# Optimization experiments

Hardware: AMD Instinct MI355X
Metric: run time of the kernel (lower is better)

Reference implementation:

```python
import jax, jax.numpy as jnp
import numpy as np

NEG_SLOPE = 0.2  # PyG GATConv leaky_relu slope


def _gat_conv(x, src, dst, W, a_s, a_d, b, H, D, concat):
    """PyG-style GATConv (eval mode, self-loops already in src/dst).
    x: [N, F_in], W: [F_in, H*D], a_s/a_d: [H, D], b: [H*D] or [D]."""
    N = x.shape[0]
    h = (x @ W).reshape(N, H, D)                      # [N, H, D]
    al_src = (h * a_s).sum(-1)                        # [N, H]
    al_dst = (h * a_d).sum(-1)                        # [N, H]
    e = jax.nn.leaky_relu(al_src[src] + al_dst[dst], NEG_SLOPE)   # [E, H]
    m = jax.ops.segment_max(e, dst, num_segments=N)               # [N, H]
    m = jnp.where(jnp.isfinite(m), m, 0.0)
    ex = jnp.exp(e - m[dst])
    denom = jax.ops.segment_sum(ex, dst, num_segments=N)
    alpha = ex / (denom[dst] + 1e-16)                 # edge softmax per dst node
    out = jax.ops.segment_sum(alpha[:, :, None] * h[src], dst, num_segments=N)  # [N, H, D]
    out = out.reshape(N, H * D) if concat else out.mean(axis=1)
    return out + b


def setup_inputs() -> dict:
    key = jax.random.key(0)
    ks = jax.random.split(key, 14)
    N, E, F_in, H, D, OUT = 50000, 800000, 256, 8, 32, 64
    g = lambda k, shape, fan: (jax.random.normal(k, shape, jnp.float32) / np.float32(np.sqrt(fan)))
    return {
        "x": jax.random.normal(ks[0], (N, F_in), jnp.float32),
        "edge_index": jax.random.randint(ks[1], (2, E), 0, N),
        # conv0: GATConv(256 -> 32, heads=8, concat)
        "W0": g(ks[2], (F_in, H * D), F_in),
        "a_src0": g(ks[3], (H, D), D),
        "a_dst0": g(ks[4], (H, D), D),
        "b0": jnp.zeros((H * D,), jnp.float32),
        # residual0: Linear(256 -> 256)
        "Wr0": g(ks[5], (F_in, H * D), F_in),
        "br0": jnp.zeros((H * D,), jnp.float32),
        # conv1: GATConv(256 -> 64, heads=1, concat=False)
        "W1": g(ks[6], (H * D, OUT), H * D),
        "a_src1": g(ks[7], (1, OUT), OUT),
        "a_dst1": g(ks[8], (1, OUT), OUT),
        "b1": jnp.zeros((OUT,), jnp.float32),
        # residual1: Linear(256 -> 64)
        "Wr1": g(ks[9], (H * D, OUT), H * D),
        "br1": jnp.zeros((OUT,), jnp.float32),
    }


def reference(x, edge_index, W0, a_src0, a_dst0, b0, Wr0, br0, W1, a_src1, a_dst1, b1, Wr1, br1):
    N = x.shape[0]
    loops = jnp.arange(N, dtype=edge_index.dtype)
    src = jnp.concatenate([edge_index[0], loops])   # add self loops
    dst = jnp.concatenate([edge_index[1], loops])
    # layer 0: GATConv + residual + ELU (dropout is identity in eval)
    h = _gat_conv(x, src, dst, W0, a_src0, a_dst0, b0, 8, 32, True)
    h = jax.nn.elu(h + (x @ Wr0 + br0))
    # final layer: heads=1, concat=False, + residual
    out = _gat_conv(h, src, dst, W1, a_src1, a_dst1, b1, 1, 64, False)
    out = out + (h @ Wr1 + br1)
    return jax.nn.log_softmax(out, axis=1)
```

## Files before the change

kernel.cpp:

```cpp
#include <hip/hip_runtime.h>
#include <math.h>

#define NEG_SLOPE 0.2f
#define BSH 7
#define NBLK_PART 256

typedef __attribute__((ext_vector_type(8))) short bf16x8;
typedef __attribute__((ext_vector_type(4))) float f32x4;
typedef __attribute__((ext_vector_type(2))) float f32x2;
typedef __attribute__((ext_vector_type(8))) unsigned short ushort8;
typedef __attribute__((ext_vector_type(4))) unsigned short ushort4v;

__device__ __forceinline__ float b2f(unsigned short u){
  return __uint_as_float(((unsigned)u) << 16);
}
__device__ __forceinline__ unsigned short f2b(float f){
  unsigned u = __float_as_uint(f);
  return (unsigned short)((u + 0x7FFFu + ((u >> 16) & 1u)) >> 16);
}

#if __has_builtin(__builtin_amdgcn_cvt_pk_f32_fp8) && __has_builtin(__builtin_amdgcn_cvt_pk_fp8_f32)
#define HW_FP8 1
#else
#define HW_FP8 0
#endif

#if !HW_FP8
__device__ __forceinline__ unsigned enc8_one(float f){
  unsigned bits = __float_as_uint(f);
  unsigned s = bits >> 31;
  unsigned e = (bits >> 23) & 255;
  unsigned mant = bits & 0x7FFFFF;
  if(e < 121){
    float af = fabsf(f);
    int m = (int)(af * 512.f + 0.5f);
    if(m > 7) m = 7;
    return (s << 7) | (unsigned)m;
  }
  unsigned lsb = (mant >> 20) & 1;
  mant += 0x7FFFF + lsb;
  if(mant >> 23){ e += 1; mant = 0; }
  unsigned m3 = mant >> 20;
  unsigned e8 = e - 120;
  if(e8 > 15 || (e8 == 15 && m3 == 7)) return (s << 7) | 0x7E;
  return (s << 7) | (e8 << 3) | m3;
}
#endif

template<bool HI>
__device__ __forceinline__ unsigned enc8_pair(float a, float b, unsigned old){
#if HW_FP8
  return __builtin_amdgcn_cvt_pk_fp8_f32(a, b, old, HI);
#else
  unsigned p = enc8_one(a) | (enc8_one(b) << 8);
  return HI ? ((old & 0x0000FFFFu) | (p << 16)) : ((old & 0xFFFF0000u) | p);
#endif
}

__device__ __forceinline__ void dec8x4v(unsigned q, f32x2& lo, f32x2& hi){
#if HW_FP8
  lo = __builtin_amdgcn_cvt_pk_f32_fp8(q, false);
  hi = __builtin_amdgcn_cvt_pk_f32_fp8(q, true);
#else
  auto dec1 = [](unsigned b)->float{
    unsigned s = (b >> 7) & 1, e = (b >> 3) & 15, m = b & 7;
    float v = (e == 0) ? (float)m * 0.001953125f
                       : __uint_as_float(((e + 120) << 23) | (m << 20));
    return s ? -v : v;
  };
  lo[0] = dec1(q & 255); lo[1] = dec1((q >> 8) & 255);
  hi[0] = dec1((q >> 16) & 255); hi[1] = dec1(q >> 24);
#endif
}

extern "C" __global__ void k_part1(const int* __restrict__ dsts, int E, int N,
                                   int NBUCK, int* __restrict__ bcnt,
                                   int* __restrict__ blockbase){
  __shared__ int hist[512];
  int blk = blockIdx.x, tid = threadIdx.x;
  for(int b = tid; b < NBUCK; b += 256) hist[b] = 0;
  __syncthreads();
  int ET = E + N;
  int chunk = (ET + NBLK_PART - 1)/NBLK_PART;
  int s0 = blk*chunk, s1 = s0+chunk < ET ? s0+chunk : ET;
  for(int e = s0+tid; e < s1; e += 256){
    int d = (e < E) ? dsts[e] : e - E;
    atomicAdd(&hist[d >> BSH], 1);
  }
  __syncthreads();
  for(int b = tid; b < NBUCK; b += 256)
    blockbase[(size_t)blk*NBUCK + b] = atomicAdd(&bcnt[b], hist[b]);
}

extern "C" __global__ void k_bscan(const int* __restrict__ bcnt, int* __restrict__ boffs,
                                   int* __restrict__ offs_last, int NBUCK, int ET){
  __shared__ int sc[512], orig[512];
  int t = threadIdx.x;
  int v = (t < NBUCK) ? bcnt[t] : 0;
  sc[t] = v; orig[t] = v;
  __syncthreads();
  for(int st=1; st<512; st<<=1){
    int u = (t >= st) ? sc[t-st] : 0;
    __syncthreads();
    sc[t] += u;
    __syncthreads();
  }
  if(t < NBUCK) boffs[t] = sc[t] - orig[t];
  if(t == 0){ boffs[NBUCK] = ET; *offs_last = ET; }
}

extern "C" __global__ void k_part2(const int* __restrict__ srcs, const int* __restrict__ dsts,
                                   int E, int N, int NBUCK,
                                   const int* __restrict__ boffs, const int* __restrict__ blockbase,
                                   uint2* __restrict__ pairs){
  __shared__ int cur[512];
  int blk = blockIdx.x, tid = threadIdx.x;
  for(int b = tid; b < NBUCK; b += 256)
    cur[b] = boffs[b] + blockbase[(size_t)blk*NBUCK + b];
  __syncthreads();
  int ET = E + N;
  int chunk = (ET + NBLK_PART - 1)/NBLK_PART;
  int s0 = blk*chunk, s1 = s0+chunk < ET ? s0+chunk : ET;
  for(int e = s0+tid; e < s1; e += 256){
    int s, d;
    if(e < E){ s = srcs[e]; d = dsts[e]; } else { s = d = e - E; }
    int pos = atomicAdd(&cur[d >> BSH], 1);
    uint2 pr; pr.x = (unsigned)d; pr.y = (unsigned)s;
    pairs[pos] = pr;
  }
}

extern "C" __global__ void k_bcsr(const uint2* __restrict__ pairs, const int* __restrict__ boffs,
                                  int N, int* __restrict__ offs, int* __restrict__ csr){
  __shared__ int hist[128], sc[128], lcur[128];
  int b = blockIdx.x, tid = threadIdx.x;
  int node0 = b << BSH;
  int base = boffs[b], endp = boffs[b+1];
  if(tid < 128) hist[tid] = 0;
  __syncthreads();
  for(int i = base + tid; i < endp; i += 256)
    atomicAdd(&hist[pairs[i].x & 127], 1);
  __syncthreads();
  if(tid < 128) sc[tid] = hist[tid];
  __syncthreads();
  for(int st=1; st<128; st<<=1){
    int u = (tid < 128 && tid >= st) ? sc[tid-st] : 0;
    __syncthreads();
    if(tid < 128) sc[tid] += u;
    __syncthreads();
  }
  if(tid < 128){
    int ex = sc[tid] - hist[tid];
    lcur[tid] = ex;
    int n = node0 + tid;
    if(n < N) offs[n] = base + ex;
  }
  __syncthreads();
  for(int i = base + tid; i < endp; i += 256){
    uint2 pr = pairs[i];
    int pos = atomicAdd(&lcur[pr.x & 127], 1);
    csr[base + pos] = (int)pr.y;
  }
}

extern "C" __global__ void k_wt2(const float* __restrict__ W0, const float* __restrict__ Wr0,
                                 const float* __restrict__ W1, const float* __restrict__ Wr1,
                                 unsigned short* __restrict__ WT0, unsigned short* __restrict__ WT1){
  int idx = blockIdx.x*256 + threadIdx.x;
  const int tot0 = 512*256;
  if(idx < tot0){
    int n = idx >> 8, k = idx & 255;
    const float* W = (n < 256) ? W0 : Wr0;
    int c = (n < 256) ? n : n - 256;
    WT0[idx] = f2b(W[(size_t)k*256 + c]);
  } else {
    idx -= tot0;
    if(idx >= 128*256) return;
    int n = idx >> 8, k = idx & 255;
    const float* W = (n < 64) ? W1 : Wr1;
    int c = (n < 64) ? n : n - 64;
    WT1[idx] = f2b(W[(size_t)k*64 + c]);
  }
}

__launch_bounds__(256)
extern "C" __global__ void k_mgemm(const unsigned short* __restrict__ A,
                                   const float* __restrict__ Afp,
                                   const unsigned short* __restrict__ WT,
                                   unsigned short* __restrict__ C, int M,
                                   int MB, int NCB, int mode,
                                   unsigned char* __restrict__ qout,
                                   unsigned short* __restrict__ rout,
                                   const float* __restrict__ as0v, const float* __restrict__ ad0v,
                                   float* __restrict__ alsout, float* __restrict__ aldout){
  int id = blockIdx.x;
  int row_blk, col_blk;
  if(NCB == 4){
    int group = id >> 5;
    int r8 = id & 7;
    col_blk = (id >> 3) & 3;
    row_blk = group*8 + r8;
  } else {
    row_blk = id; col_blk = 0;
  }
  if(row_blk >= MB) return;

  __shared__ unsigned short SH[128*128];
  unsigned short* As = SH;
  unsigned short* Bs = SH + 128*64;
  int t = threadIdx.x;
  int lane = t & 63, wid = t >> 6;
  int wr = wid >> 1, wc = wid & 1;
  int row0 = row_blk*128, col0 = col_blk*128;
  f32x4 acc[4][4] = {};

  float4 v0s[4], v1s[4];
  const float* abase[4];
  if(Afp){
    #pragma unroll
    for(int i=0; i<4; i++){
      int t2 = i*256 + t;
      int r = t2 >> 3;
      int dslot = (t2 & 7) ^ (r & 7);
      int gr = row0 + r; if(gr >= M) gr = M - 1;
      abase[i] = Afp + (size_t)gr*256 + dslot*8;
      v0s[i] = *(const float4*)(abase[i]);
      v1s[i] = *(const float4*)(abase[i] + 4);
    }
  }

  for(int k0 = 0; k0 < 256; k0 += 64){
    if(Afp){
      #pragma unroll
      for(int i=0; i<4; i++){
        ushort8 o;
        o[0]=f2b(v0s[i].x); o[1]=f2b(v0s[i].y); o[2]=f2b(v0s[i].z); o[3]=f2b(v0s[i].w);
        o[4]=f2b(v1s[i].x); o[5]=f2b(v1s[i].y); o[6]=f2b(v1s[i].z); o[7]=f2b(v1s[i].w);
        *(ushort8*)(As + i*2048 + wid*512 + lane*8) = o;
      }
    } else {
      #pragma unroll
      for(int i=0; i<4; i++){
        int t2 = i*256 + t;
        int r = t2 >> 3;
        int dslot = (t2 & 7) ^ (r & 7);
        int gr = row0 + r; if(gr >= M) gr = M - 1;
        const unsigned short* ga = A + (size_t)gr*256 + k0 + dslot*8;
        __builtin_amdgcn_global_load_lds((const __attribute__((address_space(1))) unsigned*)ga,
            (__attribute__((address_space(3))) unsigned*)(As + i*2048 + wid*512), 16, 0, 0);
      }
    }
    #pragma unroll
    for(int i=0; i<4; i++){
      int t2 = i*256 + t;
      int r = t2 >> 3;
      int dslot = (t2 & 7) ^ (r & 7);
      const unsigned short* gb = WT + (size_t)(col0 + r)*256 + k0 + dslot*8;
      __builtin_amdgcn_global_load_lds((const __attribute__((address_space(1))) unsigned*)gb,
          (__attribute__((address_space(3))) unsigned*)(Bs + i*2048 + wid*512), 16, 0, 0);
    }
    __syncthreads();
    if(Afp && k0 < 192){
      #pragma unroll
      for(int i=0; i<4; i++){
        v0s[i] = *(const float4*)(abase[i] + k0 + 64);
        v1s[i] = *(const float4*)(abase[i] + k0 + 68);
      }
    }
    #pragma unroll
    for(int kc=0; kc<2; kc++){
      bf16x8 a[4], b[4];
      int kb = kc*4 + (lane >> 4);
      #pragma unroll
      for(int f=0; f<4; f++){
        int ar = wr*64 + f*16 + (lane & 15);
        a[f] = *(const bf16x8*)&As[ar*64 + ((kb ^ (ar & 7))*8)];
        int br = wc*64 + f*16 + (lane & 15);
        b[f] = *(const bf16x8*)&Bs[br*64 + ((kb ^ (br & 7))*8)];
      }
      #pragma unroll
      for(int fm=0; fm<4; fm++)
        #pragma unroll
        for(int fn=0; fn<4; fn++)
          acc[fm][fn] = __builtin_amdgcn_mfma_f32_16x16x32_bf16(a[fm], b[fn], acc[fm][fn], 0, 0, 0);
    }
    __syncthreads();
  }

  #pragma unroll
  for(int fm=0; fm<4; fm++){
    int rl = wr*64 + fm*16 + ((lane>>4)<<2);
    #pragma unroll
    for(int r=0; r<4; r++)
      #pragma unroll
      for(int fn=0; fn<4; fn++)
        SH[(rl+r)*128 + wc*64 + (lane&15) + fn*16] = f2b(acc[fm][fn][r]);
  }
  __syncthreads();

  int cg = t & 15;
  if(mode == 0){
    bool attn = col_blk < 2;
    int colbase = col0 + cg*8;
    float4 as_lo, as_hi, ad_lo, ad_hi;
    if(attn){
      as_lo = *(const float4*)(as0v + colbase);
      as_hi = *(const float4*)(as0v + colbase + 4);
      ad_lo = *(const float4*)(ad0v + colbase);
      ad_hi = *(const float4*)(ad0v + colbase + 4);
    }
    #pragma unroll
    for(int it=0; it<8; it++){
      int rl = it*16 + (t>>4);
      int row = row0 + rl;
      ushort8 vr = *(ushort8*)&SH[rl*128 + cg*8];
      if(attn){
        float f0=b2f(vr[0]),f1=b2f(vr[1]),f2=b2f(vr[2]),f3=b2f(vr[3]);
        float f4=b2f(vr[4]),f5=b2f(vr[5]),f6=b2f(vr[6]),f7=b2f(vr[7]);
        float sd = f0*as_lo.x+f1*as_lo.y+f2*as_lo.z+f3*as_lo.w
                 + f4*as_hi.x+f5*as_hi.y+f6*as_hi.z+f7*as_hi.w;
        float dd = f0*ad_lo.x+f1*ad_lo.y+f2*ad_lo.z+f3*ad_lo.w
                 + f4*ad_hi.x+f5*ad_hi.y+f6*ad_hi.z+f7*ad_hi.w;
        sd += __shfl_xor(sd,1); sd += __shfl_xor(sd,2);
        dd += __shfl_xor(dd,1); dd += __shfl_xor(dd,2);
        uint2 q;
        q.x = enc8_pair<false>(f0,f1,0u); q.x = enc8_pair<true>(f2,f3,q.x);
        q.y = enc8_pair<false>(f4,f5,0u); q.y = enc8_pair<true>(f6,f7,q.y);
        if(row < M){
          *(uint2*)(qout + (size_t)row*256 + colbase) = q;
          if((lane&3)==0){
            int head = colbase >> 5;
            alsout[row*8 + head] = sd;
            aldout[row*8 + head] = dd;
          }
        }
      } else {
        if(row < M)
          *(ushort8*)(rout + (size_t)row*256 + (colbase - 256)) = vr;
      }
    }
  } else {
    #pragma unroll
    for(int it=0; it<8; it++){
      int rl = it*16 + (t>>4);
      int row = row0 + rl;
      ushort8 vr = *(ushort8*)&SH[rl*128 + cg*8];
      if(row < M){
        *(ushort8*)(C + (size_t)row*128 + cg*8) = vr;
        if(cg < 8){
          float f0=b2f(vr[0]),f1=b2f(vr[1]),f2=b2f(vr[2]),f3=b2f(vr[3]);
          float f4=b2f(vr[4]),f5=b2f(vr[5]),f6=b2f(vr[6]),f7=b2f(vr[7]);
          uint2 q;
          q.x = enc8_pair<false>(f0,f1,0u); q.x = enc8_pair<true>(f2,f3,q.x);
          q.y = enc8_pair<false>(f4,f5,0u); q.y = enc8_pair<true>(f6,f7,q.y);
          *(uint2*)(qout + (size_t)row*64 + cg*8) = q;
        }
      }
    }
  }
}

__launch_bounds__(256)
extern "C" __global__ void k_gather0(const unsigned short* __restrict__ r0b,
                                     const unsigned char* __restrict__ h0q,
                                     const float* __restrict__ als0, const float* __restrict__ ald0,
                                     const int* __restrict__ offs, const int* __restrict__ csr,
                                     const float* __restrict__ b0, const float* __restrict__ br0,
                                     unsigned short* __restrict__ h1b, int N){
  int n = blockIdx.x*4 + (threadIdx.x >> 6);
  if(n >= N) return;
  int lane = threadIdx.x & 63;
  int hh = lane & 7;
  int es = lane >> 3;
  int h  = es;
  int c  = lane*4;
  float ald_h = ald0[n*8 + hh];
  int beg = offs[n], end = offs[n+1];

  f32x2 A01 = {0.f, 0.f}, A23 = {0.f, 0.f};
  float den = 0.f;

  for(int chunk = beg; chunk < end; chunk += 8){
    int m = end - chunk; if(m > 8) m = 8;
    bool e_ok = es < m;
    int s = e_ok ? csr[chunk + es] : 0;
    float p = 0.f;
    if(e_ok){
      float v = als0[s*8 + hh] + ald_h;
      v = v > 0.f ? v : NEG_SLOPE*v;
      p = expf(v);
    }
    den += p;
    int sj[8]; float pj[8];
    #pragma unroll
    for(int j=0; j<8; j++){
      sj[j] = __shfl(s, j*8);
      pj[j] = __shfl(p, j*8 + h);
    }
    unsigned q[8];
    #pragma unroll
    for(int j=0; j<8; j++)
      q[j] = *(const unsigned*)(h0q + (size_t)sj[j]*256 + c);
    #pragma unroll
    for(int j=0; j<8; j++){
      f32x2 lo, hi, pv;
      dec8x4v(q[j], lo, hi);
      pv[0] = pj[j]; pv[1] = pj[j];
      A01 += pv*lo; A23 += pv*hi;
    }
  }

  den += __shfl_xor(den, 8);
  den += __shfl_xor(den, 16);
  den += __shfl_xor(den, 32);
  float rden = 1.f/(den + 1e-16f);
  rden = __shfl(rden, h);

  float a0 = A01[0]*rden, a1 = A01[1]*rden, a2 = A23[0]*rden, a3 = A23[1]*rden;

  float4 bb = *(const float4*)(b0 + c);
  float4 rb = *(const float4*)(br0 + c);
  uint2 ru = *(const uint2*)(r0b + (size_t)n*256 + c);
  float o0 = a0 + bb.x + __uint_as_float(ru.x << 16)         + rb.x;
  float o1 = a1 + bb.y + __uint_as_float(ru.x & 0xFFFF0000u) + rb.y;
  float o2 = a2 + bb.z + __uint_as_float(ru.y << 16)         + rb.z;
  float o3 = a3 + bb.w + __uint_as_float(ru.y & 0xFFFF0000u) + rb.w;
  ushort4v o;
  o[0] = f2b(o0 > 0.f ? o0 : expf(o0) - 1.f);
  o[1] = f2b(o1 > 0.f ? o1 : expf(o1) - 1.f);
  o[2] = f2b(o2 > 0.f ? o2 : expf(o2) - 1.f);
  o[3] = f2b(o3 > 0.f ? o3 : expf(o3) - 1.f);
  *(ushort4v*)(h1b + (size_t)n*256 + c) = o;
}

extern "C" __global__ void k_al1(const unsigned short* __restrict__ buf1b, const float* __restrict__ as1,
                                 const float* __restrict__ ad1, float* als1, float* ald1, int N){
  int n = blockIdx.x*4 + (threadIdx.x >> 6);
  if(n >= N) return;
  int lane = threadIdx.x & 63;
  float g = b2f(buf1b[(size_t)n*128 + lane]);
  float s = g*as1[lane], d = g*ad1[lane];
  #pragma unroll
  for(int o=32; o>0; o>>=1){ s += __shfl_xor(s,o); d += __shfl_xor(d,o); }
  if(lane == 0){ als1[n] = s; ald1[n] = d; }
}

__launch_bounds__(256)
extern "C" __global__ void k_gather1(const unsigned short* __restrict__ buf1b,
                                     const unsigned char* __restrict__ g1q,
                                     const float* __restrict__ als1, const float* __restrict__ ald1,
                                     const int* __restrict__ offs, const int* __restrict__ csr,
                                     const float* __restrict__ b1, const float* __restrict__ br1,
                                     float* __restrict__ out, int N){
  int n = blockIdx.x*4 + (threadIdx.x >> 6);
  if(n >= N) return;
  int lane = threadIdx.x & 63;
  int ch4 = lane & 15;
  int es  = lane >> 4;
  int c   = ch4*4;
  int beg = offs[n], end = offs[n+1];
  float ald_n = ald1[n];

  f32x2 A01 = {0.f, 0.f}, A23 = {0.f, 0.f};
  float den = 0.f;

  for(int chunk = beg; chunk < end; chunk += 64){
    int m = end - chunk; if(m > 64) m = 64;
    int s = (lane < m) ? csr[chunk + lane] : 0;
    float p = 0.f;
    if(lane < m){
      float v = als1[s] + ald_n;
      v = v > 0.f ? v : NEG_SLOPE*v;
      p = expf(v);
    }
    den += p;
    for(int base = 0; base < m; base += 16){
      int sv[4]; float pv[4];
      #pragma unroll
      for(int i=0; i<4; i++){
        int j = base + 4*i + es;
        int jj = j & 63;
        sv[i] = __shfl(s, jj);
        pv[i] = __shfl(p, jj);
      }
      unsigned qv[4];
      #pragma unroll
      for(int i=0; i<4; i++)
        qv[i] = *(const unsigned*)(g1q + (size_t)sv[i]*64 + c);
      #pragma unroll
      for(int i=0; i<4; i++){
        f32x2 lo, hi, pp;
        dec8x4v(qv[i], lo, hi);
        pp[0] = pv[i]; pp[1] = pv[i];
        A01 += pp*lo; A23 += pp*hi;
      }
    }
  }

  A01[0] += __shfl_xor(A01[0], 16); A01[1] += __shfl_xor(A01[1], 16);
  A23[0] += __shfl_xor(A23[0], 16); A23[1] += __shfl_xor(A23[1], 16);
  A01[0] += __shfl_xor(A01[0], 32); A01[1] += __shfl_xor(A01[1], 32);
  A23[0] += __shfl_xor(A23[0], 32); A23[1] += __shfl_xor(A23[1], 32);
  #pragma unroll
  for(int o=32; o>0; o>>=1) den += __shfl_xor(den, o);
  float rden = 1.f/(den + 1e-16f);

  float4 bb = *(const float4*)(b1 + c);
  float4 rb = *(const float4*)(br1 + c);
  uint2 ru = *(const uint2*)(buf1b + (size_t)n*128 + 64 + c);
  float v0 = A01[0]*rden + bb.x + __uint_as_float(ru.x << 16)         + rb.x;
  float v1 = A01[1]*rden + bb.y + __uint_as_float(ru.x & 0xFFFF0000u) + rb.y;
  float v2 = A23[0]*rden + bb.z + __uint_as_float(ru.y << 16)         + rb.z;
  float v3 = A23[1]*rden + bb.w + __uint_as_float(ru.y & 0xFFFF0000u) + rb.w;

  float mx = fmaxf(fmaxf(v0, v1), fmaxf(v2, v3));
  #pragma unroll
  for(int o=1; o<16; o<<=1) mx = fmaxf(mx, __shfl_xor(mx, o));
  float sm = expf(v0-mx) + expf(v1-mx) + expf(v2-mx) + expf(v3-mx);
  #pragma unroll
  for(int o=1; o<16; o<<=1) sm += __shfl_xor(sm, o);
  float l = mx + logf(sm);
  if(es == 0){
    float4 ov; ov.x = v0-l; ov.y = v1-l; ov.z = v2-l; ov.w = v3-l;
    *(float4*)(out + (size_t)n*64 + c) = ov;
  }
}

extern "C" void kernel_launch(void* const* d_in, const int* in_sizes, int n_in,
                              void* d_out, int out_size, void* d_ws, size_t ws_size,
                              hipStream_t stream){
  const float* x   = (const float*)d_in[0];
  const int*   ei  = (const int*)  d_in[1];
  const float* W0  = (const float*)d_in[2];
  const float* as0 = (const float*)d_in[3];
  const float* ad0 = (const float*)d_in[4];
  const float* b0  = (const float*)d_in[5];
  const float* Wr0 = (const float*)d_in[6];
  const float* br0 = (const float*)d_in[7];
  const float* W1  = (const float*)d_in[8];
  const float* as1 = (const float*)d_in[9];
  const float* ad1 = (const float*)d_in[10];
  const float* b1  = (const float*)d_in[11];
  const float* Wr1 = (const float*)d_in[12];
  const float* br1 = (const float*)d_in[13];
  int N = in_sizes[0] / 256;
  int E = in_sizes[1] / 2;
  const int* srcs = ei;
  const int* dsts = ei + E;
  float* out = (float*)d_out;

  int ET = E + N;
  int NBUCK = (N + 127) >> BSH;

  unsigned short* r0b   = (unsigned short*)d_ws;
  unsigned char*  h0q   = (unsigned char*)(r0b + (size_t)N*256);
  unsigned short* h1b   = (unsigned short*)(h0q + (size_t)N*256);
  unsigned short* buf1b = h1b + (size_t)N*256;
  unsigned short* WT0   = buf1b + (size_t)N*128;
  unsigned short* WT1   = WT0   + 512*256;
  float*    als0 = (float*)(WT1 + 128*256);
  float*    ald0 = als0 + (size_t)N*8;
  float*    als1 = ald0 + (size_t)N*8;
  float*    ald1 = als1 + N;
  int*      offs = (int*)(ald1 + N);
  int*      bcnt = offs + N + 1;
  int*      boffs = bcnt + NBUCK;
  int*      blockbase = boffs + NBUCK + 1;
  int*      csr  = blockbase + (size_t)NBLK_PART*NBUCK;
  uint2*    pairs = (uint2*)(csr + ET);
  pairs = (uint2*)(((uintptr_t)pairs + 7) & ~(uintptr_t)7);
  unsigned char* g1q = (unsigned char*)(pairs + ET);

  hipMemsetAsync(bcnt, 0, (size_t)NBUCK*sizeof(int), stream);
  hipLaunchKernelGGL(k_part1, dim3(NBLK_PART), dim3(256), 0, stream, dsts, E, N, NBUCK, bcnt, blockbase);
  hipLaunchKernelGGL(k_bscan, dim3(1), dim3(512), 0, stream, bcnt, boffs, offs + N, NBUCK, ET);
  hipLaunchKernelGGL(k_part2, dim3(NBLK_PART), dim3(256), 0, stream, srcs, dsts, E, N, NBUCK, boffs, blockbase, pairs);
  hipLaunchKernelGGL(k_bcsr, dim3(NBUCK), dim3(256), 0, stream, pairs, boffs, N, offs, csr);

  hipLaunchKernelGGL(k_wt2, dim3((512*256+128*256+255)/256), dim3(256), 0, stream, W0, Wr0, W1, Wr1, WT0, WT1);

  int MB = (N + 127) / 128;
  int g0 = ((MB + 7) / 8) * 32;
  hipLaunchKernelGGL(k_mgemm, dim3(g0), dim3(256), 0, stream,
                     (const unsigned short*)nullptr, x, WT0,
                     (unsigned short*)nullptr, N, MB, 4, 0,
                     h0q, r0b, as0, ad0, als0, ald0);
  hipLaunchKernelGGL(k_gather0, dim3((N+3)/4), dim3(256), 0, stream, r0b, h0q, als0, ald0, offs, csr, b0, br0, h1b, N);

  hipLaunchKernelGGL(k_mgemm, dim3(MB), dim3(256), 0, stream,
                     h1b, (const float*)nullptr, WT1,
                     buf1b, N, MB, 1, 1,
                     g1q, (unsigned short*)nullptr,
                     (const float*)nullptr, (const float*)nullptr,
                     (float*)nullptr, (float*)nullptr);
  hipLaunchKernelGGL(k_al1, dim3((N+3)/4), dim3(256), 0, stream, buf1b, as1, ad1, als1, ald1, N);
  hipLaunchKernelGGL(k_gather1, dim3((N+3)/4), dim3(256), 0, stream, buf1b, g1q, als1, ald1, offs, csr, b1, br1, out, N);
}
```

Measured before the change: 181.4 us.

## Load GEMM B fragments straight to registers, shrink LDS, fuse layer-1 attention logits

The GEMM now keeps the weight (B) operand in registers, loading MFMA fragments directly from global memory with a one-step prefetch, and stages only A through a smaller LDS buffer. The epilogue is split into two halves so the output tile fits in the reduced LDS. The layer-1 attention-logit computation (k_al1) is folded into the second GEMM's epilogue, which removes one kernel launch and a re-read of buf1b. Together these aim to raise occupancy and cut LDS traffic, at the cost of more scattered global loads for B and extra barriers in the epilogue.

```diff
diff --git a/kernel.cpp b/kernel.cpp
--- a/kernel.cpp
+++ b/kernel.cpp
@@ -184,49 +184,58 @@
 }
 
 __launch_bounds__(256)
-extern "C" __global__ void k_mgemm(const unsigned short* __restrict__ A,
+extern "C" __global__ void k_mgemm(const unsigned short* __restrict__ Ab,
                                    const float* __restrict__ Afp,
                                    const unsigned short* __restrict__ WT,
                                    unsigned short* __restrict__ C, int M,
                                    int MB, int NCB, int mode,
                                    unsigned char* __restrict__ qout,
                                    unsigned short* __restrict__ rout,
-                                   const float* __restrict__ as0v, const float* __restrict__ ad0v,
+                                   const float* __restrict__ asv, const float* __restrict__ adv,
                                    float* __restrict__ alsout, float* __restrict__ aldout){
   int id = blockIdx.x;
   int row_blk, col_blk;
   if(NCB == 4){
-    int group = id >> 5;
-    int r8 = id & 7;
     col_blk = (id >> 3) & 3;
-    row_blk = group*8 + r8;
+    row_blk = (id >> 5)*8 + (id & 7);
   } else {
     row_blk = id; col_blk = 0;
   }
   if(row_blk >= MB) return;
 
-  __shared__ unsigned short SH[128*128];
+  __shared__ unsigned short SH[64*136];
   unsigned short* As = SH;
-  unsigned short* Bs = SH + 128*64;
   int t = threadIdx.x;
   int lane = t & 63, wid = t >> 6;
   int wr = wid >> 1, wc = wid & 1;
   int row0 = row_blk*128, col0 = col_blk*128;
   f32x4 acc[4][4] = {};
 
-  float4 v0s[4], v1s[4];
-  const float* abase[4];
-  if(Afp){
-    #pragma unroll
-    for(int i=0; i<4; i++){
-      int t2 = i*256 + t;
-      int r = t2 >> 3;
-      int dslot = (t2 & 7) ^ (r & 7);
-      int gr = row0 + r; if(gr >= M) gr = M - 1;
-      abase[i] = Afp + (size_t)gr*256 + dslot*8;
-      v0s[i] = *(const float4*)(abase[i]);
-      v1s[i] = *(const float4*)(abase[i] + 4);
-    }
+  float4 va0[4], va1[4];
+  bf16x8 au[4];
+  const float* afp_ptr[4];
+  const unsigned short* ab_ptr[4];
+  #pragma unroll
+  for(int i=0; i<4; i++){
+    int t2 = i*256 + t;
+    int r = t2 >> 3, dslot = (t2 & 7) ^ (r & 7);
+    int gr = row0 + r; if(gr >= M) gr = M - 1;
+    if(Afp){
+      afp_ptr[i] = Afp + (size_t)gr*256 + dslot*8;
+      va0[i] = *(const float4*)afp_ptr[i];
+      va1[i] = *(const float4*)(afp_ptr[i] + 4);
+    } else {
+      ab_ptr[i] = Ab + (size_t)gr*256 + dslot*8;
+      au[i] = *(const bf16x8*)ab_ptr[i];
+    }
+  }
+  bf16x8 bcur[4], bnxt[4];
+  const unsigned short* bptr[4];
+  #pragma unroll
+  for(int f=0; f<4; f++){
+    int br = wc*64 + f*16 + (lane & 15);
+    bptr[f] = WT + (size_t)(col0 + br)*256 + (lane >> 4)*8;
+    bcur[f] = *(const bf16x8*)bptr[f];
   }
 
   for(int k0 = 0; k0 < 256; k0 += 64){
@@ -234,126 +243,147 @@
       #pragma unroll
       for(int i=0; i<4; i++){
         ushort8 o;
-        o[0]=f2b(v0s[i].x); o[1]=f2b(v0s[i].y); o[2]=f2b(v0s[i].z); o[3]=f2b(v0s[i].w);
-        o[4]=f2b(v1s[i].x); o[5]=f2b(v1s[i].y); o[6]=f2b(v1s[i].z); o[7]=f2b(v1s[i].w);
-        *(ushort8*)(As + i*2048 + wid*512 + lane*8) = o;
+        o[0]=f2b(va0[i].x); o[1]=f2b(va0[i].y); o[2]=f2b(va0[i].z); o[3]=f2b(va0[i].w);
+        o[4]=f2b(va1[i].x); o[5]=f2b(va1[i].y); o[6]=f2b(va1[i].z); o[7]=f2b(va1[i].w);
+        *(ushort8*)(As + i*2048 + t*8) = o;
       }
     } else {
       #pragma unroll
-      for(int i=0; i<4; i++){
-        int t2 = i*256 + t;
-        int r = t2 >> 3;
-        int dslot = (t2 & 7) ^ (r & 7);
-        int gr = row0 + r; if(gr >= M) gr = M - 1;
-        const unsigned short* ga = A + (size_t)gr*256 + k0 + dslot*8;
-        __builtin_amdgcn_global_load_lds((const __attribute__((address_space(1))) unsigned*)ga,
-            (__attribute__((address_space(3))) unsigned*)(As + i*2048 + wid*512), 16, 0, 0);
+      for(int i=0; i<4; i++)
+        *(bf16x8*)(As + i*2048 + t*8) = au[i];
+    }
+    __syncthreads();
+    if(k0 < 192){
+      if(Afp){
+        #pragma unroll
+        for(int i=0; i<4; i++){
+          va0[i] = *(const float4*)(afp_ptr[i] + k0 + 64);
+          va1[i] = *(const float4*)(afp_ptr[i] + k0 + 68);
+        }
+      } else {
+        #pragma unroll
+        for(int i=0; i<4; i++)
+          au[i] = *(const bf16x8*)(ab_ptr[i] + k0 + 64);
       }
     }
     #pragma unroll
-    for(int i=0; i<4; i++){
-      int t2 = i*256 + t;
-      int r = t2 >> 3;
-      int dslot = (t2 & 7) ^ (r & 7);
-      const unsigned short* gb = WT + (size_t)(col0 + r)*256 + k0 + dslot*8;
-      __builtin_amdgcn_global_load_lds((const __attribute__((address_space(1))) unsigned*)gb,
-          (__attribute__((address_space(3))) unsigned*)(Bs + i*2048 + wid*512), 16, 0, 0);
-    }
-    __syncthreads();
-    if(Afp && k0 < 192){
-      #pragma unroll
-      for(int i=0; i<4; i++){
-        v0s[i] = *(const float4*)(abase[i] + k0 + 64);
-        v1s[i] = *(const float4*)(abase[i] + k0 + 68);
-      }
-    }
-    #pragma unroll
-    for(int kc=0; kc<2; kc++){
-      bf16x8 a[4], b[4];
-      int kb = kc*4 + (lane >> 4);
+    for(int f=0; f<4; f++) bnxt[f] = *(const bf16x8*)(bptr[f] + k0 + 32);
+    {
+      bf16x8 a[4]; int kb = lane >> 4;
       #pragma unroll
       for(int f=0; f<4; f++){
         int ar = wr*64 + f*16 + (lane & 15);
         a[f] = *(const bf16x8*)&As[ar*64 + ((kb ^ (ar & 7))*8)];
-        int br = wc*64 + f*16 + (lane & 15);
-        b[f] = *(const bf16x8*)&Bs[br*64 + ((kb ^ (br & 7))*8)];
       }
       #pragma unroll
       for(int fm=0; fm<4; fm++)
         #pragma unroll
         for(int fn=0; fn<4; fn++)
-          acc[fm][fn] = __builtin_amdgcn_mfma_f32_16x16x32_bf16(a[fm], b[fn], acc[fm][fn], 0, 0, 0);
-    }
-    __syncthreads();
-  }
-
+          acc[fm][fn] = __builtin_amdgcn_mfma_f32_16x16x32_bf16(a[fm], bcur[fn], acc[fm][fn], 0, 0, 0);
+    }
+    if(k0 < 192){
+      #pragma unroll
+      for(int f=0; f<4; f++) bcur[f] = *(const bf16x8*)(bptr[f] + k0 + 64);
+    }
+    {
+      bf16x8 a[4]; int kb = 4 + (lane >> 4);
+      #pragma unroll
+      for(int f=0; f<4; f++){
+        int ar = wr*64 + f*16 + (lane & 15);
+        a[f] = *(const bf16x8*)&As[ar*64 + ((kb ^ (ar & 7))*8)];
+      }
+      #pragma unroll
+      for(int fm=0; fm<4; fm++)
+        #pragma unroll
+        for(int fn=0; fn<4; fn++)
+          acc[fm][fn] = __builtin_amdgcn_mfma_f32_16x16x32_bf16(a[fm], bnxt[fn], acc[fm][fn], 0, 0, 0);
+    }
+    __syncthreads();
+  }
+
+  unsigned short* CT = SH;
+  int cg = t & 15;
   #pragma unroll
-  for(int fm=0; fm<4; fm++){
-    int rl = wr*64 + fm*16 + ((lane>>4)<<2);
-    #pragma unroll
-    for(int r=0; r<4; r++)
-      #pragma unroll
-      for(int fn=0; fn<4; fn++)
-        SH[(rl+r)*128 + wc*64 + (lane&15) + fn*16] = f2b(acc[fm][fn][r]);
-  }
-  __syncthreads();
-
-  int cg = t & 15;
-  if(mode == 0){
-    bool attn = col_blk < 2;
-    int colbase = col0 + cg*8;
-    float4 as_lo, as_hi, ad_lo, ad_hi;
-    if(attn){
-      as_lo = *(const float4*)(as0v + colbase);
-      as_hi = *(const float4*)(as0v + colbase + 4);
-      ad_lo = *(const float4*)(ad0v + colbase);
-      ad_hi = *(const float4*)(ad0v + colbase + 4);
-    }
-    #pragma unroll
-    for(int it=0; it<8; it++){
-      int rl = it*16 + (t>>4);
-      int row = row0 + rl;
-      ushort8 vr = *(ushort8*)&SH[rl*128 + cg*8];
+  for(int half=0; half<2; half++){
+    __syncthreads();
+    if(wr == half){
+      #pragma unroll
+      for(int fm=0; fm<4; fm++){
+        int rbase = fm*16 + ((lane>>4)<<2);
+        #pragma unroll
+        for(int r=0; r<4; r++)
+          #pragma unroll
+          for(int fn=0; fn<4; fn++)
+            CT[(rbase+r)*136 + wc*64 + (lane&15) + fn*16] = f2b(acc[fm][fn][r]);
+      }
+    }
+    __syncthreads();
+    if(mode == 0){
+      bool attn = col_blk < 2;
+      int colbase = col0 + cg*8;
+      float4 as_lo, as_hi, ad_lo, ad_hi;
       if(attn){
-        float f0=b2f(vr[0]),f1=b2f(vr[1]),f2=b2f(vr[2]),f3=b2f(vr[3]);
-        float f4=b2f(vr[4]),f5=b2f(vr[5]),f6=b2f(vr[6]),f7=b2f(vr[7]);
-        float sd = f0*as_lo.x+f1*as_lo.y+f2*as_lo.z+f3*as_lo.w
-                 + f4*as_hi.x+f5*as_hi.y+f6*as_hi.z+f7*as_hi.w;
-        float dd = f0*ad_lo.x+f1*ad_lo.y+f2*ad_lo.z+f3*ad_lo.w
-                 + f4*ad_hi.x+f5*ad_hi.y+f6*ad_hi.z+f7*ad_hi.w;
-        sd += __shfl_xor(sd,1); sd += __shfl_xor(sd,2);
-        dd += __shfl_xor(dd,1); dd += __shfl_xor(dd,2);
-        uint2 q;
-        q.x = enc8_pair<false>(f0,f1,0u); q.x = enc8_pair<true>(f2,f3,q.x);
-        q.y = enc8_pair<false>(f4,f5,0u); q.y = enc8_pair<true>(f6,f7,q.y);
-        if(row < M){
-          *(uint2*)(qout + (size_t)row*256 + colbase) = q;
-          if((lane&3)==0){
-            int head = colbase >> 5;
-            alsout[row*8 + head] = sd;
-            aldout[row*8 + head] = dd;
-          }
-        }
-      } else {
-        if(row < M)
-          *(ushort8*)(rout + (size_t)row*256 + (colbase - 256)) = vr;
-      }
-    }
-  } else {
-    #pragma unroll
-    for(int it=0; it<8; it++){
-      int rl = it*16 + (t>>4);
-      int row = row0 + rl;
-      ushort8 vr = *(ushort8*)&SH[rl*128 + cg*8];
-      if(row < M){
-        *(ushort8*)(C + (size_t)row*128 + cg*8) = vr;
-        if(cg < 8){
+        as_lo = *(const float4*)(asv + colbase);
+        as_hi = *(const float4*)(asv + colbase + 4);
+        ad_lo = *(const float4*)(adv + colbase);
+        ad_hi = *(const float4*)(adv + colbase + 4);
+      }
+      #pragma unroll
+      for(int it=0; it<4; it++){
+        int rl = it*16 + (t>>4);
+        int row = row0 + half*64 + rl;
+        ushort8 vr = *(ushort8*)&CT[rl*136 + cg*8];
+        if(attn){
           float f0=b2f(vr[0]),f1=b2f(vr[1]),f2=b2f(vr[2]),f3=b2f(vr[3]);
           float f4=b2f(vr[4]),f5=b2f(vr[5]),f6=b2f(vr[6]),f7=b2f(vr[7]);
+          float sd = f0*as_lo.x+f1*as_lo.y+f2*as_lo.z+f3*as_lo.w
+                   + f4*as_hi.x+f5*as_hi.y+f6*as_hi.z+f7*as_hi.w;
+          float dd = f0*ad_lo.x+f1*ad_lo.y+f2*ad_lo.z+f3*ad_lo.w
+                   + f4*ad_hi.x+f5*ad_hi.y+f6*ad_hi.z+f7*ad_hi.w;
+          sd += __shfl_xor(sd,1); sd += __shfl_xor(sd,2);
+          dd += __shfl_xor(dd,1); dd += __shfl_xor(dd,2);
           uint2 q;
           q.x = enc8_pair<false>(f0,f1,0u); q.x = enc8_pair<true>(f2,f3,q.x);
           q.y = enc8_pair<false>(f4,f5,0u); q.y = enc8_pair<true>(f6,f7,q.y);
-          *(uint2*)(qout + (size_t)row*64 + cg*8) = q;
+          if(row < M){
+            *(uint2*)(qout + (size_t)row*256 + colbase) = q;
+            if((t&3)==0){
+              int head = colbase >> 5;
+              alsout[row*8 + head] = sd;
+              aldout[row*8 + head] = dd;
+            }
+          }
+        } else {
+          if(row < M)
+            *(ushort8*)(rout + (size_t)row*256 + (colbase - 256)) = vr;
+        }
+      }
+    } else {
+      #pragma unroll
+      for(int it=0; it<4; it++){
+        int rl = it*16 + (t>>4);
+        int row = row0 + half*64 + rl;
+        ushort8 vr = *(ushort8*)&CT[rl*136 + cg*8];
+        if(row < M){
+          *(ushort8*)(C + (size_t)row*128 + cg*8) = vr;
+          if(cg < 8){
+            float f0=b2f(vr[0]),f1=b2f(vr[1]),f2=b2f(vr[2]),f3=b2f(vr[3]);
+            float f4=b2f(vr[4]),f5=b2f(vr[5]),f6=b2f(vr[6]),f7=b2f(vr[7]);
+            uint2 q;
+            q.x = enc8_pair<false>(f0,f1,0u); q.x = enc8_pair<true>(f2,f3,q.x);
+            q.y = enc8_pair<false>(f4,f5,0u); q.y = enc8_pair<true>(f6,f7,q.y);
+            *(uint2*)(qout + (size_t)row*64 + cg*8) = q;
+            float sd = f0*asv[cg*8+0]+f1*asv[cg*8+1]+f2*asv[cg*8+2]+f3*asv[cg*8+3]
+                     + f4*asv[cg*8+4]+f5*asv[cg*8+5]+f6*asv[cg*8+6]+f7*asv[cg*8+7];
+            float dd = f0*adv[cg*8+0]+f1*adv[cg*8+1]+f2*adv[cg*8+2]+f3*adv[cg*8+3]
+                     + f4*adv[cg*8+4]+f5*adv[cg*8+5]+f6*adv[cg*8+6]+f7*adv[cg*8+7];
+            sd += __shfl_xor(sd,1); sd += __shfl_xor(sd,2); sd += __shfl_xor(sd,4);
+            dd += __shfl_xor(dd,1); dd += __shfl_xor(dd,2); dd += __shfl_xor(dd,4);
+            if((t&15)==0){
+              alsout[row] = sd;
+              aldout[row] = dd;
+            }
+          }
         }
       }
     }
@@ -431,18 +461,6 @@
   o[2] = f2b(o2 > 0.f ? o2 : expf(o2) - 1.f);
   o[3] = f2b(o3 > 0.f ? o3 : expf(o3) - 1.f);
   *(ushort4v*)(h1b + (size_t)n*256 + c) = o;
-}
-
-extern "C" __global__ void k_al1(const unsigned short* __restrict__ buf1b, const float* __restrict__ as1,
-                                 const float* __restrict__ ad1, float* als1, float* ald1, int N){
-  int n = blockIdx.x*4 + (threadIdx.x >> 6);
-  if(n >= N) return;
-  int lane = threadIdx.x & 63;
-  float g = b2f(buf1b[(size_t)n*128 + lane]);
-  float s = g*as1[lane], d = g*ad1[lane];
-  #pragma unroll
-  for(int o=32; o>0; o>>=1){ s += __shfl_xor(s,o); d += __shfl_xor(d,o); }
-  if(lane == 0){ als1[n] = s; ald1[n] = d; }
 }
 
 __launch_bounds__(256)
@@ -591,8 +609,6 @@
                      h1b, (const float*)nullptr, WT1,
                      buf1b, N, MB, 1, 1,
                      g1q, (unsigned short*)nullptr,
-                     (const float*)nullptr, (const float*)nullptr,
-                     (float*)nullptr, (float*)nullptr);
-  hipLaunchKernelGGL(k_al1, dim3((N+3)/4), dim3(256), 0, stream, buf1b, as1, ad1, als1, ald1, N);
+                     as1, ad1, als1, ald1);
   hipLaunchKernelGGL(k_gather1, dim3((N+3)/4), dim3(256), 0, stream, buf1b, g1q, als1, ald1, offs, csr, b1, br1, out, N);
 }
```

Result: slower. 196.9 us (+8.5%).
